# Kernel tuning notes

Hardware: AMD Instinct MI355X
Metric: run time of the kernel (lower is better)

Reference implementation:

```python
import jax, jax.numpy as jnp
import numpy as np

HEAD_NUM = 16
QKV_DIM = 16
EMB = 256
MS_HID = 16
B, R, C = 4, 512, 512


def setup_inputs() -> dict:
    key = jax.random.key(0)
    ks = jax.random.split(key, 10)
    inv = 1.0 / np.sqrt(EMB)
    m1 = np.sqrt(0.5)
    m2 = np.sqrt(1.0 / 16.0)
    return {
        "row_emb": jax.random.normal(ks[0], (B, R, EMB), jnp.float32),
        "col_emb": jax.random.normal(ks[1], (B, C, EMB), jnp.float32),
        "cost_mat": jax.random.uniform(ks[2], (B, R, C), jnp.float32),
        # Linear(no bias) weights stored as [in, out] so y = x @ W
        "Wq": jax.random.uniform(ks[3], (EMB, HEAD_NUM * QKV_DIM), jnp.float32, -inv, inv),
        "Wk": jax.random.uniform(ks[4], (EMB, HEAD_NUM * QKV_DIM), jnp.float32, -inv, inv),
        "Wv": jax.random.uniform(ks[5], (EMB, HEAD_NUM * QKV_DIM), jnp.float32, -inv, inv),
        "mix1_weight": jax.random.uniform(ks[6], (HEAD_NUM, 2, MS_HID), jnp.float32, -m1, m1),
        "mix1_bias": jax.random.uniform(ks[7], (HEAD_NUM, MS_HID), jnp.float32, -m1, m1),
        "mix2_weight": jax.random.uniform(ks[8], (HEAD_NUM, MS_HID, 1), jnp.float32, -m2, m2),
        "mix2_bias": jax.random.uniform(ks[9], (HEAD_NUM, 1), jnp.float32, -m2, m2),
    }


def _split_heads(x):
    # [b, g, h*s] -> [b, h, g, s]
    b, g, _ = x.shape
    return x.reshape(b, g, HEAD_NUM, QKV_DIM).transpose(0, 2, 1, 3)


def reference(row_emb, col_emb, cost_mat, Wq, Wk, Wv, mix1_weight, mix1_bias, mix2_weight, mix2_bias):
    q = _split_heads(row_emb @ Wq)  # [b,h,r,s]
    k = _split_heads(col_emb @ Wk)  # [b,h,c,s]
    v = _split_heads(col_emb @ Wv)  # [b,h,c,s]

    dot = jnp.einsum("bhrs,bhcs->bhrc", q, k) / jnp.sqrt(jnp.float32(QKV_DIM))
    cost = jnp.broadcast_to(cost_mat[:, None, :, :], dot.shape)
    two = jnp.stack((dot, cost), axis=-1)  # [b,h,r,c,2]

    # per-head 2-layer MLP applied to each (row, col) score pair
    ms1 = jnp.einsum("bhrcx,hxm->bhrcm", two, mix1_weight) + mix1_bias[None, :, None, None, :]
    ms1 = jax.nn.relu(ms1)
    mixed = jnp.einsum("bhrcm,hmo->bhrco", ms1, mix2_weight)[..., 0] + mix2_bias[None, :, None, None, 0]

    weights = jax.nn.softmax(mixed, axis=3)  # [b,h,r,c]
    out = jnp.einsum("bhrc,bhcs->bhrs", weights, v)
    b, h, r, s = out.shape
    return out.transpose(0, 2, 1, 3).reshape(b, r, h * s)
```

## Files before the change

kernel.cpp:

```cpp
#include <hip/hip_runtime.h>

#define NB 4
#define NH 16
#define RR 512
#define CC 512
#define EMB 256
#define SD 16
#define MH 16

typedef __attribute__((ext_vector_type(8))) short short8;
typedef __attribute__((ext_vector_type(4))) float f32x4;
typedef __attribute__((ext_vector_type(4))) unsigned short ushort4v;

__device__ __forceinline__ float bf2f(unsigned short s) {
  unsigned u = ((unsigned)s) << 16;
  return __builtin_bit_cast(float, u);
}
__device__ __forceinline__ unsigned short f2bf(float f) {
  unsigned u = __builtin_bit_cast(unsigned, f);
  u = u + 0x7FFFu + ((u >> 16) & 1u);
  return (unsigned short)(u >> 16);
}

__global__ __launch_bounds__(64) void transpose_w(
    const float* __restrict__ Wq, const float* __restrict__ Wk,
    const float* __restrict__ Wv, unsigned short* __restrict__ WT) {
  const float* src = (blockIdx.x == 0) ? Wq : (blockIdx.x == 1) ? Wk : Wv;
  unsigned short* dst = WT + blockIdx.x * (EMB * EMB);
  int n = blockIdx.y;
  int e0 = threadIdx.x * 4;
  ushort4v v;
  v.x = f2bf(src[(e0 + 0) * EMB + n]);
  v.y = f2bf(src[(e0 + 1) * EMB + n]);
  v.z = f2bf(src[(e0 + 2) * EMB + n]);
  v.w = f2bf(src[(e0 + 3) * EMB + n]);
  *(ushort4v*)(dst + n * EMB + e0) = v;
}

__global__ __launch_bounds__(256) void proj_kernel(
    const float* __restrict__ rowe, const float* __restrict__ cole,
    const unsigned short* __restrict__ WT,
    unsigned short* __restrict__ Q, unsigned short* __restrict__ K,
    unsigned short* __restrict__ VT) {
  int tid = threadIdx.x;
  int wid = tid >> 6, lane = tid & 63, l15 = lane & 15, quad = lane >> 4;
  int wt = blockIdx.x * 4 + wid;
  int mat = wt >> 11;
  int t = wt & 2047;
  int rt = t >> 4;
  int nt = t & 15;
  const float* X = (mat == 0) ? rowe : cole;
  const unsigned short* Wm = WT + mat * (EMB * EMB);

  const short8* ap = (const short8*)(Wm + (nt * 16 + l15) * EMB + quad * 8);
  const float* xrow = X + (size_t)(rt * 16 + l15) * EMB + quad * 8;
  f32x4 acc = {0.f, 0.f, 0.f, 0.f};
#pragma unroll
  for (int e = 0; e < 8; ++e) {
    short8 af = ap[e * 4];
    f32x4 b0 = *(const f32x4*)(xrow + e * 32);
    f32x4 b1 = *(const f32x4*)(xrow + e * 32 + 4);
    short8 bf;
#pragma unroll
    for (int j = 0; j < 4; ++j) {
      ((unsigned short*)&bf)[j]     = f2bf(b0[j]);
      ((unsigned short*)&bf)[j + 4] = f2bf(b1[j]);
    }
    acc = __builtin_amdgcn_mfma_f32_16x16x32_bf16(af, bf, acc, 0, 0, 0);
  }
  int row = rt * 16 + l15;
  int b = row >> 9, loc = row & 511;
  if (mat < 2) {
    unsigned short* dst = ((mat == 0) ? Q : K) +
        ((size_t)((b * NH + nt) * 512 + loc) * SD + quad * 4);
    ushort4v pk;
    pk.x = f2bf(acc[0]); pk.y = f2bf(acc[1]); pk.z = f2bf(acc[2]); pk.w = f2bf(acc[3]);
    *(ushort4v*)dst = pk;
  } else {
#pragma unroll
    for (int i = 0; i < 4; ++i)
      VT[(size_t)((b * NH + nt) * SD + quad * 4 + i) * CC + loc] = f2bf(acc[i]);
  }
}

__global__ __launch_bounds__(256) void attn_kernel(
    const unsigned short* __restrict__ Q, const unsigned short* __restrict__ K,
    const unsigned short* __restrict__ VT, const float* __restrict__ cost,
    const float* __restrict__ m1w, const float* __restrict__ m1b,
    const float* __restrict__ m2w, const float* __restrict__ m2b,
    float* __restrict__ out) {
  __shared__ alignas(16) unsigned short Psh[4][16 * 512];
  int tid = threadIdx.x;
  int wid = tid >> 6, lane = tid & 63, l15 = lane & 15, quad = lane >> 4;
  int rb = blockIdx.x, h = blockIdx.y, b = blockIdx.z;
  int bh = b * NH + h;
  int r0 = rb * 64 + wid * 16;

  float wa[MH], wc[MH], wd[MH], we[MH];
#pragma unroll
  for (int m = 0; m < MH; ++m) {
    wa[m] = m1w[(h * 2 + 0) * MH + m] * 0.25f;
    wc[m] = m1w[(h * 2 + 1) * MH + m];
    wd[m] = m1b[h * MH + m];
    we[m] = m2w[h * MH + m];
  }
  float wb2 = m2b[h];

  short8 qf = {0, 0, 0, 0, 0, 0, 0, 0};
  const unsigned short* Qb = Q + (size_t)bh * RR * SD;
  if (quad < 2) qf = *(const short8*)(Qb + (r0 + l15) * SD + quad * 8);

  const unsigned short* Kb = K + (size_t)bh * CC * SD;
  const float* crow = cost + ((size_t)b * RR + r0 + l15) * CC;
  unsigned short* psrow = &Psh[wid][l15 * 512];

  float mrun = -1e30f;
  for (int ct = 0; ct < CC; ct += 16) {
    short8 kf = {0, 0, 0, 0, 0, 0, 0, 0};
    if (quad < 2) kf = *(const short8*)(Kb + (ct + l15) * SD + quad * 8);
    f32x4 acc = {0.f, 0.f, 0.f, 0.f};
    acc = __builtin_amdgcn_mfma_f32_16x16x32_bf16(kf, qf, acc, 0, 0, 0);
    int c0 = ct + quad * 4;
    f32x4 cf = *(const f32x4*)(crow + c0);
    ushort4v pk;
#pragma unroll
    for (int i = 0; i < 4; ++i) {
      float x = acc[i];
      float s = wb2;
#pragma unroll
      for (int m = 0; m < MH; ++m) {
        float t1 = fmaf(wc[m], cf[i], wd[m]);
        t1 = fmaf(wa[m], x, t1);
        t1 = fmaxf(t1, 0.f);
        s = fmaf(we[m], t1, s);
      }
      mrun = fmaxf(mrun, s);
      ((unsigned short*)&pk)[i] = f2bf(s);
    }
    int g = ((c0 >> 3) ^ (l15 & 7));
    *(ushort4v*)(psrow + g * 8 + (c0 & 7)) = pk;
  }
  mrun = fmaxf(mrun, __shfl_xor(mrun, 16));
  mrun = fmaxf(mrun, __shfl_xor(mrun, 32));

  const unsigned short* vb = VT + ((size_t)bh * SD + l15) * CC;
  f32x4 o = {0.f, 0.f, 0.f, 0.f};
  float lsum = 0.f;
  const float LOG2E = 1.44269504088896f;
  float mb2 = mrun * LOG2E;
  for (int ct = 0; ct < CC; ct += 32) {
    int c0 = ct + quad * 8;
    int g = ((c0 >> 3) ^ (l15 & 7));
    short8 praw = *(const short8*)(psrow + g * 8);
    short8 pf;
#pragma unroll
    for (int j = 0; j < 8; ++j) {
      float x = bf2f((unsigned short)((unsigned short*)&praw)[j]);
      float p = exp2f(fmaf(x, LOG2E, -mb2));
      lsum += p;
      ((unsigned short*)&pf)[j] = (short)f2bf(p);
    }
    short8 vf = *(const short8*)(vb + c0);
    o = __builtin_amdgcn_mfma_f32_16x16x32_bf16(pf, vf, o, 0, 0, 0);
  }
  lsum += __shfl_xor(lsum, 16);
  lsum += __shfl_xor(lsum, 32);

#pragma unroll
  for (int i = 0; i < 4; ++i) {
    float li = __shfl(lsum, quad * 4 + i);
    out[((size_t)b * RR + r0 + quad * 4 + i) * (NH * SD) + h * SD + l15] = o[i] / li;
  }
}

extern "C" void kernel_launch(void* const* d_in, const int* in_sizes, int n_in,
                              void* d_out, int out_size, void* d_ws, size_t ws_size,
                              hipStream_t stream) {
  const float* rowe = (const float*)d_in[0];
  const float* cole = (const float*)d_in[1];
  const float* cost = (const float*)d_in[2];
  const float* Wq   = (const float*)d_in[3];
  const float* Wk   = (const float*)d_in[4];
  const float* Wv   = (const float*)d_in[5];
  const float* m1w  = (const float*)d_in[6];
  const float* m1b  = (const float*)d_in[7];
  const float* m2w  = (const float*)d_in[8];
  const float* m2b  = (const float*)d_in[9];
  float* outp = (float*)d_out;

  unsigned short* ws = (unsigned short*)d_ws;
  unsigned short* Qw  = ws;
  unsigned short* Kw  = ws + 524288;
  unsigned short* VTw = ws + 1048576;
  unsigned short* WTw = ws + 1572864;

  transpose_w<<<dim3(3, 256, 1), 64, 0, stream>>>(Wq, Wk, Wv, WTw);
  proj_kernel<<<dim3(1536, 1, 1), 256, 0, stream>>>(rowe, cole, WTw, Qw, Kw, VTw);
  attn_kernel<<<dim3(8, NH, NB), 256, 0, stream>>>(Qw, Kw, VTw, cost,
                                                   m1w, m1b, m2w, m2b, outp);
}
```

Before: 139.1 us.

## Split attention columns across waves, reuse projection inputs, prefetch loads, fast exp2

```diff
diff --git a/kernel.cpp b/kernel.cpp
--- a/kernel.cpp
+++ b/kernel.cpp
@@ -9,6 +9,7 @@
 #define MH 16
 
 typedef __attribute__((ext_vector_type(8))) short short8;
+typedef __attribute__((ext_vector_type(8))) unsigned short ushort8;
 typedef __attribute__((ext_vector_type(4))) float f32x4;
 typedef __attribute__((ext_vector_type(4))) unsigned short ushort4v;
 
@@ -22,19 +23,22 @@
   return (unsigned short)(u >> 16);
 }
 
-__global__ __launch_bounds__(64) void transpose_w(
+__global__ __launch_bounds__(256) void prep_w(
     const float* __restrict__ Wq, const float* __restrict__ Wk,
     const float* __restrict__ Wv, unsigned short* __restrict__ WT) {
-  const float* src = (blockIdx.x == 0) ? Wq : (blockIdx.x == 1) ? Wk : Wv;
-  unsigned short* dst = WT + blockIdx.x * (EMB * EMB);
-  int n = blockIdx.y;
-  int e0 = threadIdx.x * 4;
-  ushort4v v;
-  v.x = f2bf(src[(e0 + 0) * EMB + n]);
-  v.y = f2bf(src[(e0 + 1) * EMB + n]);
-  v.z = f2bf(src[(e0 + 2) * EMB + n]);
-  v.w = f2bf(src[(e0 + 3) * EMB + n]);
-  *(ushort4v*)(dst + n * EMB + e0) = v;
+  int bi = blockIdx.x;
+  int mat = bi >> 4, ngrp = bi & 15;
+  const float* src = (mat == 0) ? Wq : (mat == 1) ? Wk : Wv;
+  unsigned short* dst = WT + mat * (EMB * EMB);
+  int n = ngrp * 16 + (threadIdx.x >> 4);
+  int e0 = (threadIdx.x & 15) * 16;
+  ushort8 v0, v1;
+#pragma unroll
+  for (int j = 0; j < 8; ++j) v0[j] = f2bf(src[(e0 + j) * EMB + n]);
+#pragma unroll
+  for (int j = 0; j < 8; ++j) v1[j] = f2bf(src[(e0 + 8 + j) * EMB + n]);
+  *(ushort8*)(dst + n * EMB + e0) = v0;
+  *(ushort8*)(dst + n * EMB + e0 + 8) = v1;
 }
 
 __global__ __launch_bounds__(256) void proj_kernel(
@@ -45,41 +49,45 @@
   int tid = threadIdx.x;
   int wid = tid >> 6, lane = tid & 63, l15 = lane & 15, quad = lane >> 4;
   int wt = blockIdx.x * 4 + wid;
-  int mat = wt >> 11;
-  int t = wt & 2047;
-  int rt = t >> 4;
-  int nt = t & 15;
+  int mat = wt >> 9;
+  int t = wt & 511;
+  int rt = t >> 2, ng = t & 3;
   const float* X = (mat == 0) ? rowe : cole;
   const unsigned short* Wm = WT + mat * (EMB * EMB);
-
-  const short8* ap = (const short8*)(Wm + (nt * 16 + l15) * EMB + quad * 8);
   const float* xrow = X + (size_t)(rt * 16 + l15) * EMB + quad * 8;
-  f32x4 acc = {0.f, 0.f, 0.f, 0.f};
+
+  short8 xf[8];
 #pragma unroll
   for (int e = 0; e < 8; ++e) {
-    short8 af = ap[e * 4];
     f32x4 b0 = *(const f32x4*)(xrow + e * 32);
     f32x4 b1 = *(const f32x4*)(xrow + e * 32 + 4);
-    short8 bf;
 #pragma unroll
     for (int j = 0; j < 4; ++j) {
-      ((unsigned short*)&bf)[j]     = f2bf(b0[j]);
-      ((unsigned short*)&bf)[j + 4] = f2bf(b1[j]);
-    }
-    acc = __builtin_amdgcn_mfma_f32_16x16x32_bf16(af, bf, acc, 0, 0, 0);
+      ((unsigned short*)&xf[e])[j]     = f2bf(b0[j]);
+      ((unsigned short*)&xf[e])[j + 4] = f2bf(b1[j]);
+    }
   }
   int row = rt * 16 + l15;
   int b = row >> 9, loc = row & 511;
-  if (mat < 2) {
-    unsigned short* dst = ((mat == 0) ? Q : K) +
-        ((size_t)((b * NH + nt) * 512 + loc) * SD + quad * 4);
-    ushort4v pk;
-    pk.x = f2bf(acc[0]); pk.y = f2bf(acc[1]); pk.z = f2bf(acc[2]); pk.w = f2bf(acc[3]);
-    *(ushort4v*)dst = pk;
-  } else {
-#pragma unroll
-    for (int i = 0; i < 4; ++i)
-      VT[(size_t)((b * NH + nt) * SD + quad * 4 + i) * CC + loc] = f2bf(acc[i]);
+#pragma unroll
+  for (int hh = 0; hh < 4; ++hh) {
+    int nt = ng * 4 + hh;
+    const short8* ap = (const short8*)(Wm + (nt * 16 + l15) * EMB + quad * 8);
+    f32x4 acc = {0.f, 0.f, 0.f, 0.f};
+#pragma unroll
+    for (int e = 0; e < 8; ++e)
+      acc = __builtin_amdgcn_mfma_f32_16x16x32_bf16(ap[e * 4], xf[e], acc, 0, 0, 0);
+    if (mat < 2) {
+      ushort4v pk;
+      pk.x = f2bf(acc[0]); pk.y = f2bf(acc[1]); pk.z = f2bf(acc[2]); pk.w = f2bf(acc[3]);
+      unsigned short* dst = ((mat == 0) ? Q : K) +
+          ((size_t)((b * NH + nt) * 512 + loc) * SD + quad * 4);
+      *(ushort4v*)dst = pk;
+    } else {
+#pragma unroll
+      for (int i = 0; i < 4; ++i)
+        VT[(size_t)((b * NH + nt) * SD + quad * 4 + i) * CC + loc] = f2bf(acc[i]);
+    }
   }
 }
 
@@ -89,12 +97,16 @@
     const float* __restrict__ m1w, const float* __restrict__ m1b,
     const float* __restrict__ m2w, const float* __restrict__ m2b,
     float* __restrict__ out) {
-  __shared__ alignas(16) unsigned short Psh[4][16 * 512];
+  __shared__ alignas(16) unsigned short Psh[4][16 * 256];
+  __shared__ float Osh[2][256];
+  __shared__ float MLsh[2][2][2][16];
   int tid = threadIdx.x;
   int wid = tid >> 6, lane = tid & 63, l15 = lane & 15, quad = lane >> 4;
+  int rt = wid >> 1, ch = wid & 1;
   int rb = blockIdx.x, h = blockIdx.y, b = blockIdx.z;
   int bh = b * NH + h;
-  int r0 = rb * 64 + wid * 16;
+  int r0 = rb * 32 + rt * 16;
+  int cbase = ch * 256;
 
   float wa[MH], wc[MH], wd[MH], we[MH];
 #pragma unroll
@@ -110,18 +122,24 @@
   const unsigned short* Qb = Q + (size_t)bh * RR * SD;
   if (quad < 2) qf = *(const short8*)(Qb + (r0 + l15) * SD + quad * 8);
 
-  const unsigned short* Kb = K + (size_t)bh * CC * SD;
-  const float* crow = cost + ((size_t)b * RR + r0 + l15) * CC;
-  unsigned short* psrow = &Psh[wid][l15 * 512];
+  const unsigned short* Kb = K + ((size_t)bh * CC + cbase) * SD;
+  const float* crow = cost + ((size_t)b * RR + r0 + l15) * CC + cbase;
+  unsigned short* psrow = &Psh[wid][l15 * 256];
 
   float mrun = -1e30f;
-  for (int ct = 0; ct < CC; ct += 16) {
-    short8 kf = {0, 0, 0, 0, 0, 0, 0, 0};
-    if (quad < 2) kf = *(const short8*)(Kb + (ct + l15) * SD + quad * 8);
+  short8 kf_c = {0, 0, 0, 0, 0, 0, 0, 0};
+  if (quad < 2) kf_c = *(const short8*)(Kb + l15 * SD + quad * 8);
+  f32x4 cf_c = *(const f32x4*)(crow + quad * 4);
+#pragma unroll 4
+  for (int it = 0; it < 16; ++it) {
+    int itn = (it + 1) & 15;
+    short8 kf_n = {0, 0, 0, 0, 0, 0, 0, 0};
+    if (quad < 2) kf_n = *(const short8*)(Kb + (itn * 16 + l15) * SD + quad * 8);
+    f32x4 cf_n = *(const f32x4*)(crow + itn * 16 + quad * 4);
+
     f32x4 acc = {0.f, 0.f, 0.f, 0.f};
-    acc = __builtin_amdgcn_mfma_f32_16x16x32_bf16(kf, qf, acc, 0, 0, 0);
-    int c0 = ct + quad * 4;
-    f32x4 cf = *(const f32x4*)(crow + c0);
+    acc = __builtin_amdgcn_mfma_f32_16x16x32_bf16(kf_c, qf, acc, 0, 0, 0);
+    int c0 = it * 16 + quad * 4;
     ushort4v pk;
 #pragma unroll
     for (int i = 0; i < 4; ++i) {
@@ -129,7 +147,7 @@
       float s = wb2;
 #pragma unroll
       for (int m = 0; m < MH; ++m) {
-        float t1 = fmaf(wc[m], cf[i], wd[m]);
+        float t1 = fmaf(wc[m], cf_c[i], wd[m]);
         t1 = fmaf(wa[m], x, t1);
         t1 = fmaxf(t1, 0.f);
         s = fmaf(we[m], t1, s);
@@ -139,37 +157,59 @@
     }
     int g = ((c0 >> 3) ^ (l15 & 7));
     *(ushort4v*)(psrow + g * 8 + (c0 & 7)) = pk;
+    kf_c = kf_n; cf_c = cf_n;
   }
   mrun = fmaxf(mrun, __shfl_xor(mrun, 16));
   mrun = fmaxf(mrun, __shfl_xor(mrun, 32));
 
-  const unsigned short* vb = VT + ((size_t)bh * SD + l15) * CC;
+  const unsigned short* vb = VT + ((size_t)bh * SD + l15) * CC + cbase;
   f32x4 o = {0.f, 0.f, 0.f, 0.f};
   float lsum = 0.f;
-  const float LOG2E = 1.44269504088896f;
-  float mb2 = mrun * LOG2E;
-  for (int ct = 0; ct < CC; ct += 32) {
-    int c0 = ct + quad * 8;
-    int g = ((c0 >> 3) ^ (l15 & 7));
-    short8 praw = *(const short8*)(psrow + g * 8);
+  const float L2E = 1.44269504088896f;
+  float mb2 = mrun * L2E;
+  short8 vf_c = *(const short8*)(vb + quad * 8);
+  int g0 = ((quad * 8) >> 3) ^ (l15 & 7);
+  short8 pr_c = *(const short8*)(psrow + g0 * 8);
+#pragma unroll
+  for (int it = 0; it < 8; ++it) {
+    int itn = (it + 1) & 7;
+    short8 vf_n = *(const short8*)(vb + itn * 32 + quad * 8);
+    int c0n = itn * 32 + quad * 8;
+    int gn = ((c0n >> 3) ^ (l15 & 7));
+    short8 pr_n = *(const short8*)(psrow + gn * 8);
     short8 pf;
 #pragma unroll
     for (int j = 0; j < 8; ++j) {
-      float x = bf2f((unsigned short)((unsigned short*)&praw)[j]);
-      float p = exp2f(fmaf(x, LOG2E, -mb2));
+      float x = bf2f(((unsigned short*)&pr_c)[j]);
+      float p = __builtin_amdgcn_exp2f(fmaf(x, L2E, -mb2));
       lsum += p;
       ((unsigned short*)&pf)[j] = (short)f2bf(p);
     }
-    short8 vf = *(const short8*)(vb + c0);
-    o = __builtin_amdgcn_mfma_f32_16x16x32_bf16(pf, vf, o, 0, 0, 0);
+    o = __builtin_amdgcn_mfma_f32_16x16x32_bf16(pf, vf_c, o, 0, 0, 0);
+    vf_c = vf_n; pr_c = pr_n;
   }
   lsum += __shfl_xor(lsum, 16);
   lsum += __shfl_xor(lsum, 32);
 
-#pragma unroll
-  for (int i = 0; i < 4; ++i) {
-    float li = __shfl(lsum, quad * 4 + i);
-    out[((size_t)b * RR + r0 + quad * 4 + i) * (NH * SD) + h * SD + l15] = o[i] / li;
+  if (quad == 0) { MLsh[rt][ch][0][l15] = mrun; MLsh[rt][ch][1][l15] = lsum; }
+  if (ch == 1) {
+#pragma unroll
+    for (int i = 0; i < 4; ++i) Osh[rt][(quad * 4 + i) * 16 + l15] = o[i];
+  }
+  __syncthreads();
+  if (ch == 0) {
+#pragma unroll
+    for (int i = 0; i < 4; ++i) {
+      int r = quad * 4 + i;
+      float m0 = MLsh[rt][0][0][r], l0 = MLsh[rt][0][1][r];
+      float m1 = MLsh[rt][1][0][r], l1 = MLsh[rt][1][1][r];
+      float M = fmaxf(m0, m1);
+      float a0 = __builtin_amdgcn_exp2f((m0 - M) * L2E);
+      float a1 = __builtin_amdgcn_exp2f((m1 - M) * L2E);
+      float l = a0 * l0 + a1 * l1;
+      float val = (a0 * o[i] + a1 * Osh[rt][r * 16 + l15]) / l;
+      out[((size_t)b * RR + r0 + r) * (NH * SD) + h * SD + l15] = val;
+    }
   }
 }
 
@@ -194,8 +234,8 @@
   unsigned short* VTw = ws + 1048576;
   unsigned short* WTw = ws + 1572864;
 
-  transpose_w<<<dim3(3, 256, 1), 64, 0, stream>>>(Wq, Wk, Wv, WTw);
-  proj_kernel<<<dim3(1536, 1, 1), 256, 0, stream>>>(rowe, cole, WTw, Qw, Kw, VTw);
-  attn_kernel<<<dim3(8, NH, NB), 256, 0, stream>>>(Qw, Kw, VTw, cost,
-                                                   m1w, m1b, m2w, m2b, outp);
-}
+  prep_w<<<dim3(48, 1, 1), 256, 0, stream>>>(Wq, Wk, Wv, WTw);
+  proj_kernel<<<dim3(384, 1, 1), 256, 0, stream>>>(rowe, cole, WTw, Qw, Kw, VTw);
+  attn_kernel<<<dim3(16, NH, NB), 256, 0, stream>>>(Qw, Kw, VTw, cost,
+                                                    m1w, m1b, m2w, m2b, outp);
+}
```

New measurement: 125.7 us. 1.11x faster.
